# Performance work log

Hardware: AMD Instinct MI355X
Metric: run time of the kernel (lower is better)

The kernel has to match this reference:

```python
import jax, jax.numpy as jnp
import numpy as np

EMBED = 2048
HEAD = 128

def setup_inputs() -> dict:
    key = jax.random.key(0)
    ks = jax.random.split(key, 7)
    s = 1.0 / np.sqrt(EMBED)
    x = jax.random.normal(ks[0], (8, 2048, EMBED), dtype=jnp.float32)
    Wq = jax.random.uniform(ks[1], (EMBED, HEAD), jnp.float32, -s, s)
    bq = jax.random.uniform(ks[2], (HEAD,), jnp.float32, -s, s)
    Wk = jax.random.uniform(ks[3], (EMBED, HEAD), jnp.float32, -s, s)
    bk = jax.random.uniform(ks[4], (HEAD,), jnp.float32, -s, s)
    Wv = jax.random.uniform(ks[5], (EMBED, HEAD), jnp.float32, -s, s)
    bv = jax.random.uniform(ks[6], (HEAD,), jnp.float32, -s, s)
    return {"x": x, "Wq": Wq, "bq": bq, "Wk": Wk, "bk": bk, "Wv": Wv, "bv": bv}

def reference(x, Wq, bq, Wk, bk, Wv, bv):
    # x: [B, T, E]
    T = x.shape[1]
    Q = x @ Wq + bq  # [B, T, H]
    K = x @ Wk + bk
    V = x @ Wv + bv
    scale = 1.0 / jnp.sqrt(jnp.float32(HEAD))
    scores = jnp.einsum('bqh,bkh->bqk', Q, K) * scale  # [B, T, T]
    causal = jnp.tril(jnp.ones((T, T), dtype=bool))
    scores = jnp.where(causal, scores, jnp.float32(-jnp.inf))
    att = jax.nn.softmax(scores, axis=-1)
    # dropout is identity in eval/reference mode
    return jnp.einsum('bqk,bkh->bqh', att, V)
```

## Files before the change

kernel.cpp:

```cpp
#include <hip/hip_runtime.h>

#define EMBED 2048
#define HEAD 128
#define BATCH 8
#define SEQ 2048

typedef __attribute__((ext_vector_type(4))) float f32x4;
typedef __attribute__((ext_vector_type(8))) __bf16 bf16x8;
typedef __attribute__((ext_vector_type(8))) short short8;

static __device__ __forceinline__ ushort f2bf(float x){
    unsigned u = __float_as_uint(x);
    u += 0x7fffu + ((u >> 16) & 1u);
    return (ushort)(u >> 16);
}

#define MFMA16(a,b,c) __builtin_amdgcn_mfma_f32_16x16x32_bf16((a),(b),(c),0,0,0)

#define GLL16(g, l) __builtin_amdgcn_global_load_lds( \
    (const __attribute__((address_space(1))) void*)(g), \
    (__attribute__((address_space(3))) void*)(l), 16, 0, 0)

__global__ __launch_bounds__(256) void prep_wt(const float* __restrict__ Wq,
                                               const float* __restrict__ Wk,
                                               const float* __restrict__ Wv,
                                               ushort* __restrict__ wt){
    __shared__ float ld[64][129];
    const int w  = blockIdx.y;
    const int k0 = blockIdx.x * 64;
    const int tid = threadIdx.x;
    const float* W = (w == 0) ? Wq : ((w == 1) ? Wk : Wv);
    #pragma unroll
    for (int ii = 0; ii < 32; ii++){
        int idx = tid + 256 * ii;
        int row = idx >> 7, col = idx & 127;
        ld[row][col] = W[(size_t)(k0 + row) * HEAD + col];
    }
    __syncthreads();
    int n  = tid >> 1;
    int kh = (tid & 1) * 32;
    __attribute__((aligned(16))) ushort tmp[32];
    #pragma unroll
    for (int ii = 0; ii < 32; ii++) tmp[ii] = f2bf(ld[kh + ii][n]);
    ushort* dst = wt + (size_t)(w * HEAD + n) * EMBED + k0 + kh;
    #pragma unroll
    for (int q = 0; q < 4; q++)
        *(short8*)(dst + q * 8) = *(const short8*)(tmp + q * 8);
}

__global__ __launch_bounds__(256, 2) void qkv_gemm(const float* __restrict__ x,
                                                   const ushort* __restrict__ wt,
                                                   const float* __restrict__ bq,
                                                   const float* __restrict__ bk,
                                                   const float* __restrict__ bv,
                                                   ushort* __restrict__ Qb,
                                                   ushort* __restrict__ Kb,
                                                   ushort* __restrict__ Vt){
    __shared__ char smem[81920];
    float* ts = (float*)smem;

    const int half  = blockIdx.x;
    const int mtile = blockIdx.y;
    const int tid   = threadIdx.x;
    const int lane  = tid & 63;
    const int wid   = tid >> 6;
    const int l15   = lane & 15, lhi = lane >> 4;
    const int xrow0 = mtile * 64;

    const ushort* wsrc_base = wt + (size_t)(half * 192) * EMBED;
    const int grow  = lane >> 3;
    const int gch   = lane & 7;
    const int xgrow = lane >> 4;
    const int xgch  = lane & 15;

    f32x4 acc[4][3];
    #pragma unroll
    for (int i = 0; i < 4; i++)
        #pragma unroll
        for (int j = 0; j < 3; j++) acc[i][j] = (f32x4){0.f,0.f,0.f,0.f};

    const int NK = EMBED / 64;

    {
        #pragma unroll
        for (int g = 0; g < 4; g++){
            int r0  = wid * 16 + g * 4;
            int row = r0 + xgrow;
            int cs  = xgch ^ (((row & 7) << 1) | ((row & 8) >> 3));
            GLL16(x + (size_t)(xrow0 + row) * EMBED + cs * 4, smem + r0 * 256);
        }
        #pragma unroll
        for (int g = 0; g < 6; g++){
            int r0  = wid * 48 + g * 8;
            int row = r0 + grow;
            GLL16(wsrc_base + (size_t)row * EMBED + ((gch ^ (row & 7)) * 8), smem + 32768 + r0 * 128);
        }
    }

    for (int kt = 0; kt < NK; ++kt){
        char* xs_c = smem + (kt & 1) * 16384;
        char* wl_c = smem + 32768 + (kt & 1) * 24576;
        char* xs_n = smem + ((kt + 1) & 1) * 16384;
        char* wl_n = smem + 32768 + ((kt + 1) & 1) * 24576;

        if (kt < NK - 1){
            const float* xsrc = x + (kt + 1) * 64;
            #pragma unroll
            for (int g = 0; g < 4; g++){
                int r0  = wid * 16 + g * 4;
                int row = r0 + xgrow;
                int cs  = xgch ^ (((row & 7) << 1) | ((row & 8) >> 3));
                GLL16(xsrc + (size_t)(xrow0 + row) * EMBED + cs * 4, xs_n + r0 * 256);
            }
            const ushort* wsrc = wsrc_base + (kt + 1) * 64;
            #pragma unroll
            for (int g = 0; g < 6; g++){
                int r0  = wid * 48 + g * 8;
                int row = r0 + grow;
                GLL16(wsrc + (size_t)row * EMBED + ((gch ^ (row & 7)) * 8), wl_n + r0 * 128);
            }
            asm volatile("s_waitcnt vmcnt(10)" ::: "memory");
        } else {
            asm volatile("s_waitcnt vmcnt(0)" ::: "memory");
        }
        __builtin_amdgcn_s_barrier();

        #pragma unroll
        for (int kc = 0; kc < 2; kc++){
            bf16x8 af[4], bfj[3];
            #pragma unroll
            for (int i = 0; i < 4; i++){
                int row = i * 16 + l15;
                int swz = ((row & 7) << 1) | ((row & 8) >> 3);
                int c0  = kc * 8 + lhi * 2;
                f32x4 lo = *(const f32x4*)(xs_c + row * 256 + ((c0    ) ^ swz) * 16);
                f32x4 hi = *(const f32x4*)(xs_c + row * 256 + ((c0 + 1) ^ swz) * 16);
                bf16x8 a;
                a[0] = (__bf16)lo[0]; a[1] = (__bf16)lo[1]; a[2] = (__bf16)lo[2]; a[3] = (__bf16)lo[3];
                a[4] = (__bf16)hi[0]; a[5] = (__bf16)hi[1]; a[6] = (__bf16)hi[2]; a[7] = (__bf16)hi[3];
                af[i] = a;
            }
            #pragma unroll
            for (int j = 0; j < 3; j++){
                int row = wid * 48 + j * 16 + l15;
                bfj[j] = *(const bf16x8*)(wl_c + row * 128 + (((kc*4 + lhi) ^ (l15 & 7)) * 16));
            }
            #pragma unroll
            for (int i = 0; i < 4; i++)
                #pragma unroll
                for (int j = 0; j < 3; j++)
                    acc[i][j] = MFMA16(af[i], bfj[j], acc[i][j]);
        }
        __builtin_amdgcn_s_barrier();
    }

    float bval[3];
    #pragma unroll
    for (int j = 0; j < 3; j++){
        int c = half * 192 + wid * 48 + j * 16 + l15;
        bval[j] = (c < 128) ? bq[c] : ((c < 256) ? bk[c - 128] : bv[c - 256]);
    }
    #pragma unroll
    for (int j = 0; j < 3; j++){
        int cb = half * 192 + wid * 48 + j * 16;
        if (cb < 256){
            ushort* dst = (cb < 128) ? Qb : Kb;
            int cl = (cb < 128) ? (cb + l15) : (cb - 128 + l15);
            #pragma unroll
            for (int i = 0; i < 4; i++)
                #pragma unroll
                for (int r = 0; r < 4; r++)
                    dst[(size_t)(mtile*64 + i*16 + lhi*4 + r) * HEAD + cl] = f2bf(acc[i][j][r] + bval[j]);
        }
    }
    if (half == 1){
        __syncthreads();
        #pragma unroll
        for (int j = 0; j < 3; j++){
            int cb = 192 + wid * 48 + j * 16;
            if (cb >= 256){
                int vc = cb - 256 + l15;
                #pragma unroll
                for (int i = 0; i < 4; i++)
                    #pragma unroll
                    for (int r = 0; r < 4; r++)
                        ts[(i*16 + lhi*4 + r) * 132 + vc] = acc[i][j][r] + bval[j];
            }
        }
        __syncthreads();
        int n  = tid >> 1;
        int mc = (tid & 1) * 32;
        int bb = mtile >> 5;
        int trow = (mtile & 31) * 64 + mc;
        __attribute__((aligned(16))) ushort tmp[32];
        #pragma unroll
        for (int ii = 0; ii < 32; ii++) tmp[ii] = f2bf(ts[(mc + ii) * 132 + n]);
        ushort* dst = Vt + ((size_t)(bb * HEAD + n)) * SEQ + trow;
        #pragma unroll
        for (int q = 0; q < 4; q++)
            *(short8*)(dst + q * 8) = *(const short8*)(tmp + q * 8);
    }
}

__global__ __launch_bounds__(256) void attn(const ushort* __restrict__ Qb,
                                            const ushort* __restrict__ Kb,
                                            const ushort* __restrict__ Vt,
                                            float* __restrict__ po,
                                            float* __restrict__ pm,
                                            float* __restrict__ pl){
    __shared__ char smem[40960];
    char* Ks = smem;
    char* Vs = smem + 16384;
    char* Ps = smem + 32768;

    const int slot = blockIdx.x;
    const int b    = blockIdx.y;
    const int qi   = slot >> 1;
    const int qt   = (b < 4) ? qi : (31 - qi);
    const int half = slot & 1;
    const int NT   = qt + 1;
    const int tmid = (NT + 1) >> 1;
    const int t0   = half ? tmid : 0;
    const int t1   = half ? NT : tmid;

    const int qb    = qt * 64;
    const int tid   = threadIdx.x;
    const int lane  = tid & 63, wid = tid >> 6;
    const int l15   = lane & 15, lhi = lane >> 4;
    const float scale = 0.08838834764831845f;

    bf16x8 qf[4];
    {
        const ushort* qp = Qb + ((size_t)(b * SEQ + qb + wid * 16 + l15)) * HEAD;
        #pragma unroll
        for (int kc = 0; kc < 4; kc++)
            qf[kc] = *(const bf16x8*)(qp + kc * 32 + lhi * 8);
    }

    f32x4 o[8];
    #pragma unroll
    for (int d = 0; d < 8; d++) o[d] = (f32x4){0.f,0.f,0.f,0.f};
    float mr[4] = {-1e30f,-1e30f,-1e30f,-1e30f};
    float lr[4] = {0.f,0.f,0.f,0.f};

    char* Pw = Ps + wid * 2048;

    const int krow = tid >> 4, kch = tid & 15;
    const int vd   = tid >> 3, vch = tid & 7;

    short8 kr[4], vr[4];
    {
        const int kvb = t0 * 64;
        #pragma unroll
        for (int j = 0; j < 4; j++)
            kr[j] = *(const short8*)(Kb + ((size_t)(b * SEQ + kvb + krow + 16*j)) * HEAD + kch * 8);
        #pragma unroll
        for (int j = 0; j < 4; j++)
            vr[j] = *(const short8*)(Vt + ((size_t)(b * HEAD + vd + 32*j)) * SEQ + kvb + vch * 8);
    }

    for (int t = t0; t < t1; ++t){
        __syncthreads();
        #pragma unroll
        for (int j = 0; j < 4; j++){
            int row = krow + 16*j;
            *(short8*)(Ks + row * 256 + ((kch ^ (row & 15)) * 16)) = kr[j];
        }
        #pragma unroll
        for (int j = 0; j < 4; j++){
            int d = vd + 32*j;
            *(short8*)(Vs + d * 128 + ((vch ^ (d & 7)) * 16)) = vr[j];
        }
        if (t + 1 < t1){
            const int kvb2 = (t + 1) * 64;
            #pragma unroll
            for (int j = 0; j < 4; j++)
                kr[j] = *(const short8*)(Kb + ((size_t)(b * SEQ + kvb2 + krow + 16*j)) * HEAD + kch * 8);
            #pragma unroll
            for (int j = 0; j < 4; j++)
                vr[j] = *(const short8*)(Vt + ((size_t)(b * HEAD + vd + 32*j)) * SEQ + kvb2 + vch * 8);
        }
        asm volatile("s_waitcnt lgkmcnt(0)" ::: "memory");
        __builtin_amdgcn_s_barrier();
        __builtin_amdgcn_sched_barrier(0);

        const int kvb = t * 64;
        f32x4 s[4];
        #pragma unroll
        for (int ns = 0; ns < 4; ns++){
            s[ns] = (f32x4){0.f,0.f,0.f,0.f};
            int row = ns * 16 + l15;
            #pragma unroll
            for (int kc = 0; kc < 4; kc++){
                int ch = (kc * 4 + lhi) ^ (row & 15);
                bf16x8 bfr = *(const bf16x8*)(Ks + row * 256 + ch * 16);
                s[ns] = MFMA16(qf[kc], bfr, s[ns]);
            }
        }

        float mx[4];
        #pragma unroll
        for (int r = 0; r < 4; r++){
            #pragma unroll
            for (int ns = 0; ns < 4; ns++){
                float v = s[ns][r] * scale;
                if (t == qt){
                    int kvg = kvb + ns * 16 + l15;
                    int qg  = qb + wid * 16 + lhi * 4 + r;
                    if (kvg > qg) v = -1e30f;
                }
                s[ns][r] = v;
            }
            float m0 = fmaxf(fmaxf(s[0][r], s[1][r]), fmaxf(s[2][r], s[3][r]));
            m0 = fmaxf(m0, __shfl_xor(m0, 1));
            m0 = fmaxf(m0, __shfl_xor(m0, 2));
            m0 = fmaxf(m0, __shfl_xor(m0, 4));
            m0 = fmaxf(m0, __shfl_xor(m0, 8));
            mx[r] = m0;
        }
        float alpha[4];
        #pragma unroll
        for (int r = 0; r < 4; r++){
            float mn = fmaxf(mr[r], mx[r]);
            alpha[r] = __expf(mr[r] - mn);
            mr[r] = mn;
            float sum = 0.f;
            #pragma unroll
            for (int ns = 0; ns < 4; ns++){
                float p = __expf(s[ns][r] - mn);
                s[ns][r] = p;
                sum += p;
            }
            sum += __shfl_xor(sum, 1);
            sum += __shfl_xor(sum, 2);
            sum += __shfl_xor(sum, 4);
            sum += __shfl_xor(sum, 8);
            lr[r] = lr[r] * alpha[r] + sum;
        }
        #pragma unroll
        for (int d = 0; d < 8; d++)
            #pragma unroll
            for (int r = 0; r < 4; r++) o[d][r] *= alpha[r];

        #pragma unroll
        for (int ns = 0; ns < 4; ns++)
            #pragma unroll
            for (int r = 0; r < 4; r++){
                int row = lhi * 4 + r;
                int byteoff = row * 128 + (((ns * 16 + l15) * 2) ^ ((row & 7) << 4));
                *(ushort*)(Pw + byteoff) = f2bf(s[ns][r]);
            }
        asm volatile("s_waitcnt lgkmcnt(0)" ::: "memory");
        __builtin_amdgcn_sched_barrier(0);

        #pragma unroll
        for (int kc = 0; kc < 2; kc++){
            int abyte = l15 * 128 + ((kc * 64 + lhi * 16) ^ ((l15 & 7) << 4));
            bf16x8 af = *(const bf16x8*)(Pw + abyte);
            #pragma unroll
            for (int ds = 0; ds < 8; ds++){
                int drow = ds * 16 + l15;
                int bbyte = drow * 128 + ((kc * 64 + lhi * 16) ^ ((drow & 7) << 4));
                bf16x8 bfr = *(const bf16x8*)(Vs + bbyte);
                o[ds] = MFMA16(af, bfr, o[ds]);
            }
        }
    }

    float* pob = po + ((size_t)half * 16384 + (size_t)b * SEQ) * HEAD;
    #pragma unroll
    for (int r = 0; r < 4; r++){
        int q = qb + wid * 16 + lhi * 4 + r;
        #pragma unroll
        for (int ds = 0; ds < 8; ds++)
            pob[(size_t)q * HEAD + ds * 16 + l15] = o[ds][r];
        if (l15 == 0){
            pm[half * 16384 + b * SEQ + q] = mr[r];
            pl[half * 16384 + b * SEQ + q] = lr[r];
        }
    }
}

__global__ __launch_bounds__(256) void merge(const float* __restrict__ po,
                                             const float* __restrict__ pm,
                                             const float* __restrict__ pl,
                                             float* __restrict__ out){
    int g = blockIdx.x * 256 + threadIdx.x;
    int row = g >> 2;
    int dq  = (g & 3) * 32;
    float m0 = pm[row], m1 = pm[16384 + row];
    float l0 = pl[row], l1 = pl[16384 + row];
    float M  = fmaxf(m0, m1);
    float w0 = __expf(m0 - M), w1 = __expf(m1 - M);
    float inv = 1.0f / (w0 * l0 + w1 * l1);
    const float4* p0 = (const float4*)(po + (size_t)row * HEAD + dq);
    const float4* p1 = (const float4*)(po + (size_t)(16384 + row) * HEAD + dq);
    float4* op = (float4*)(out + (size_t)row * HEAD + dq);
    #pragma unroll
    for (int i = 0; i < 8; i++){
        float4 a = p0[i], c = p1[i];
        float4 r;
        r.x = (w0*a.x + w1*c.x) * inv;
        r.y = (w0*a.y + w1*c.y) * inv;
        r.z = (w0*a.z + w1*c.z) * inv;
        r.w = (w0*a.w + w1*c.w) * inv;
        op[i] = r;
    }
}

extern "C" void kernel_launch(void* const* d_in, const int* in_sizes, int n_in,
                              void* d_out, int out_size, void* d_ws, size_t ws_size,
                              hipStream_t stream){
    const float* x  = (const float*)d_in[0];
    const float* Wq = (const float*)d_in[1];
    const float* bq = (const float*)d_in[2];
    const float* Wk = (const float*)d_in[3];
    const float* bk = (const float*)d_in[4];
    const float* Wv = (const float*)d_in[5];
    const float* bv = (const float*)d_in[6];
    float* out = (float*)d_out;

    char* ws = (char*)d_ws;
    ushort* Qb = (ushort*)ws;
    ushort* Kb = (ushort*)(ws + (size_t)4  * 1024 * 1024);
    ushort* Vt = (ushort*)(ws + (size_t)8  * 1024 * 1024);
    ushort* Wt = (ushort*)(ws + (size_t)12 * 1024 * 1024);
    float*  po = (float*) (ws + (size_t)14 * 1024 * 1024);
    float*  pm = (float*) (ws + (size_t)31 * 1024 * 1024);
    float*  pl = (float*) (ws + (size_t)31 * 1024 * 1024 + 262144);

    prep_wt <<<dim3(32, 3), 256, 0, stream>>>(Wq, Wk, Wv, Wt);
    qkv_gemm<<<dim3(2, 256), 256, 0, stream>>>(x, Wt, bq, bk, bv, Qb, Kb, Vt);
    attn    <<<dim3(64, 8), 256, 0, stream>>>(Qb, Kb, Vt, po, pm, pl);
    merge   <<<256, 256, 0, stream>>>(po, pm, pl, out);
}
```

Measured before the change: 121.4 us.

## Use triple-buffered K=32 pipeline in QKV GEMM with prefetch depth two

The QKV projection GEMM now loads K-tiles of 32 instead of 64 and keeps three LDS buffers, prefetching two tiles ahead instead of one. Shared memory per block drops from 80KB to 60KB, and the swizzle patterns and staging index math are rewritten for the narrower tiles. The aim is to hide global-load latency better with a deeper pipeline. The cost is twice as many iterations and barriers per tile, with fewer MFMAs issued between each barrier.

After: 122.9 us. No clear change (+1.2%).

```diff
diff --git a/kernel.cpp b/kernel.cpp
--- a/kernel.cpp
+++ b/kernel.cpp
@@ -56,7 +56,7 @@
                                                    ushort* __restrict__ Qb,
                                                    ushort* __restrict__ Kb,
                                                    ushort* __restrict__ Vt){
-    __shared__ char smem[81920];
+    __shared__ char smem[61440];
     float* ts = (float*)smem;
 
     const int half  = blockIdx.x;
@@ -68,10 +68,7 @@
     const int xrow0 = mtile * 64;
 
     const ushort* wsrc_base = wt + (size_t)(half * 192) * EMBED;
-    const int grow  = lane >> 3;
-    const int gch   = lane & 7;
-    const int xgrow = lane >> 4;
-    const int xgch  = lane & 15;
+    const int NK = EMBED / 32;
 
     f32x4 acc[4][3];
     #pragma unroll
@@ -79,80 +76,71 @@
         #pragma unroll
         for (int j = 0; j < 3; j++) acc[i][j] = (f32x4){0.f,0.f,0.f,0.f};
 
-    const int NK = EMBED / 64;
-
-    {
-        #pragma unroll
-        for (int g = 0; g < 4; g++){
-            int r0  = wid * 16 + g * 4;
-            int row = r0 + xgrow;
-            int cs  = xgch ^ (((row & 7) << 1) | ((row & 8) >> 3));
-            GLL16(x + (size_t)(xrow0 + row) * EMBED + cs * 4, smem + r0 * 256);
-        }
-        #pragma unroll
-        for (int g = 0; g < 6; g++){
-            int r0  = wid * 48 + g * 8;
-            int row = r0 + grow;
-            GLL16(wsrc_base + (size_t)row * EMBED + ((gch ^ (row & 7)) * 8), smem + 32768 + r0 * 128);
-        }
-    }
+    #define STAGE(KT, B) do{                                                           \
+        const float*  xsrc = x + (size_t)xrow0 * EMBED + (KT) * 32;                    \
+        const ushort* wsrc = wsrc_base + (KT) * 32;                                    \
+        char* xb = smem + (B) * 8192;                                                  \
+        char* wb = smem + 24576 + (B) * 12288;                                         \
+        _Pragma("unroll")                                                              \
+        for (int g = 0; g < 2; g++){                                                   \
+            int c   = tid + 256 * g;                                                   \
+            int row = c >> 3, ch = c & 7;                                              \
+            int cs  = ch ^ (row & 7);                                                  \
+            GLL16(xsrc + (size_t)row * EMBED + cs * 4, xb + c * 16);                   \
+        }                                                                              \
+        _Pragma("unroll")                                                              \
+        for (int g = 0; g < 3; g++){                                                   \
+            int c   = tid + 256 * g;                                                   \
+            int row = c >> 2, ch = c & 3;                                              \
+            int cs  = ch ^ (row & 3);                                                  \
+            GLL16(wsrc + (size_t)row * EMBED + cs * 8, wb + c * 16);                   \
+        }                                                                              \
+    } while(0)
+
+    STAGE(0, 0);
+    STAGE(1, 1);
 
     for (int kt = 0; kt < NK; ++kt){
-        char* xs_c = smem + (kt & 1) * 16384;
-        char* wl_c = smem + 32768 + (kt & 1) * 24576;
-        char* xs_n = smem + ((kt + 1) & 1) * 16384;
-        char* wl_n = smem + 32768 + ((kt + 1) & 1) * 24576;
-
-        if (kt < NK - 1){
-            const float* xsrc = x + (kt + 1) * 64;
-            #pragma unroll
-            for (int g = 0; g < 4; g++){
-                int r0  = wid * 16 + g * 4;
-                int row = r0 + xgrow;
-                int cs  = xgch ^ (((row & 7) << 1) | ((row & 8) >> 3));
-                GLL16(xsrc + (size_t)(xrow0 + row) * EMBED + cs * 4, xs_n + r0 * 256);
-            }
-            const ushort* wsrc = wsrc_base + (kt + 1) * 64;
-            #pragma unroll
-            for (int g = 0; g < 6; g++){
-                int r0  = wid * 48 + g * 8;
-                int row = r0 + grow;
-                GLL16(wsrc + (size_t)row * EMBED + ((gch ^ (row & 7)) * 8), wl_n + r0 * 128);
-            }
+        const int bc = kt % 3;
+        if (kt + 2 < NK){
+            STAGE(kt + 2, (kt + 2) % 3);
             asm volatile("s_waitcnt vmcnt(10)" ::: "memory");
+        } else if (kt + 2 == NK){
+            asm volatile("s_waitcnt vmcnt(5)" ::: "memory");
         } else {
             asm volatile("s_waitcnt vmcnt(0)" ::: "memory");
         }
         __builtin_amdgcn_s_barrier();
 
-        #pragma unroll
-        for (int kc = 0; kc < 2; kc++){
-            bf16x8 af[4], bfj[3];
-            #pragma unroll
-            for (int i = 0; i < 4; i++){
-                int row = i * 16 + l15;
-                int swz = ((row & 7) << 1) | ((row & 8) >> 3);
-                int c0  = kc * 8 + lhi * 2;
-                f32x4 lo = *(const f32x4*)(xs_c + row * 256 + ((c0    ) ^ swz) * 16);
-                f32x4 hi = *(const f32x4*)(xs_c + row * 256 + ((c0 + 1) ^ swz) * 16);
-                bf16x8 a;
-                a[0] = (__bf16)lo[0]; a[1] = (__bf16)lo[1]; a[2] = (__bf16)lo[2]; a[3] = (__bf16)lo[3];
-                a[4] = (__bf16)hi[0]; a[5] = (__bf16)hi[1]; a[6] = (__bf16)hi[2]; a[7] = (__bf16)hi[3];
-                af[i] = a;
-            }
-            #pragma unroll
-            for (int j = 0; j < 3; j++){
-                int row = wid * 48 + j * 16 + l15;
-                bfj[j] = *(const bf16x8*)(wl_c + row * 128 + (((kc*4 + lhi) ^ (l15 & 7)) * 16));
-            }
-            #pragma unroll
-            for (int i = 0; i < 4; i++)
-                #pragma unroll
-                for (int j = 0; j < 3; j++)
-                    acc[i][j] = MFMA16(af[i], bfj[j], acc[i][j]);
-        }
+        char* xs_c = smem + bc * 8192;
+        char* wl_c = smem + 24576 + bc * 12288;
+        bf16x8 af[4], bfj[3];
+        #pragma unroll
+        for (int i = 0; i < 4; i++){
+            int row = i * 16 + l15;
+            int swz = row & 7;
+            int c0  = lhi * 2;
+            f32x4 lo = *(const f32x4*)(xs_c + row * 128 + ((c0    ) ^ swz) * 16);
+            f32x4 hi = *(const f32x4*)(xs_c + row * 128 + ((c0 + 1) ^ swz) * 16);
+            bf16x8 a;
+            a[0] = (__bf16)lo[0]; a[1] = (__bf16)lo[1]; a[2] = (__bf16)lo[2]; a[3] = (__bf16)lo[3];
+            a[4] = (__bf16)hi[0]; a[5] = (__bf16)hi[1]; a[6] = (__bf16)hi[2]; a[7] = (__bf16)hi[3];
+            af[i] = a;
+        }
+        #pragma unroll
+        for (int j = 0; j < 3; j++){
+            int row = wid * 48 + j * 16 + l15;
+            bfj[j] = *(const bf16x8*)(wl_c + row * 64 + ((lhi ^ (row & 3)) * 16));
+        }
+        #pragma unroll
+        for (int i = 0; i < 4; i++)
+            #pragma unroll
+            for (int j = 0; j < 3; j++)
+                acc[i][j] = MFMA16(af[i], bfj[j], acc[i][j]);
+
         __builtin_amdgcn_s_barrier();
     }
+    #undef STAGE
 
     float bval[3];
     #pragma unroll
```
